# Performance work log

Hardware: AMD Instinct MI355X
Metric: run time of the kernel (lower is better)

Reference implementation:

```python
import jax, jax.numpy as jnp
import numpy as np

N = 1048576  # n_envs (patients)

# param column order in the (N,30) params array
_P = ['BW','KMAX','B','D','KMIN','KABS','F','KP1','KP2','KP3','FSNC','KE1','KE2',
     'K1','K2','VM0','VMX','KM0','M1','M2','M4','KA1','KA2','VI','P2U','IB','KI',
     'M30','KD','KSC']
_IDX = {n: i for i, n in enumerate(_P)}


def setup_inputs() -> dict:
    key = jax.random.key(0)
    ks = jax.random.split(key, 6)
    # positive, well-conditioned values (B < 1, divisors bounded away from 0)
    x = jax.random.uniform(ks[0], (N, 13), jnp.float32, 0.1, 2.0)
    params = jax.random.uniform(ks[1], (N, 30), jnp.float32, 0.5, 0.95)
    action_ins = jax.random.uniform(ks[2], (N, 1), jnp.float32, 0.0, 1.0)
    action_CHO = jax.random.uniform(ks[3], (N, 1), jnp.float32, 0.0, 1.0)
    last_Qsto = jax.random.uniform(ks[4], (N, 1), jnp.float32, 0.0, 1.0)
    last_foodtaken = jax.random.uniform(ks[5], (N, 1), jnp.float32, 0.0, 1.0)
    return {'x': x, 'params': params, 'action_ins': action_ins,
            'action_CHO': action_CHO, 'last_Qsto': last_Qsto,
            'last_foodtaken': last_foodtaken}


def _dxdt(x, params, action_ins, action_CHO, last_Qsto, last_foodtaken):
    p = lambda n: params[:, _IDX[n]:_IDX[n] + 1]  # (N,1) column
    xs = [x[:, i:i + 1] for i in range(13)]

    BW = p('BW'); KMAX = p('KMAX'); B = p('B'); D = p('D'); KMIN = p('KMIN')
    KABS = p('KABS'); F = p('F'); KP1 = p('KP1'); KP2 = p('KP2'); KP3 = p('KP3')
    FSNC = p('FSNC'); KE1 = p('KE1'); KE2 = p('KE2'); K1 = p('K1'); K2 = p('K2')
    VM0 = p('VM0'); VMX = p('VMX'); KM0 = p('KM0'); M1 = p('M1'); M2 = p('M2')
    M4 = p('M4'); KA1 = p('KA1'); KA2 = p('KA2'); VI = p('VI'); P2U = p('P2U')
    IB = p('IB'); KI = p('KI'); M30 = p('M30'); KD = p('KD'); KSC = p('KSC')

    f_insulin = action_ins * 6000.0 / BW
    qsto = xs[0] + xs[1]
    Dbar = last_Qsto + last_foodtaken

    dx0 = -KMAX * xs[0] + action_CHO * 1000.0

    aa = 5.0 / 2.0 / (1.0 - B) / (Dbar + 1e-7)
    cc = 5.0 / 2.0 / D / (Dbar + 1e-7)
    kgut_true = KMIN + (KMAX - KMIN) / 2.0 * (
        jnp.tanh(aa * (qsto - B * Dbar)) - jnp.tanh(cc * (qsto - D * Dbar)) + 2.0)
    kgut = jnp.where(Dbar > 0, kgut_true, KMAX)

    dx1 = KMAX * xs[0] - xs[1] * kgut
    dx2 = kgut * xs[1] - KABS * xs[2]

    Rat = F * KABS * xs[2] / BW
    EGPt = KP1 - KP2 * xs[3] - KP3 * xs[8]
    Et = jnp.where(xs[3] > KE2, KE1 * (xs[3] - KE2), 0.0)
    dx3 = jnp.maximum(EGPt, 0.0) + Rat - FSNC - Et - K1 * xs[3] + K2 * xs[4]
    dx3 = jnp.where(xs[3] >= 0, dx3, 0.0)

    Vmt = VM0 + VMX * xs[6]
    Uidt = Vmt * xs[4] / (KM0 + xs[4])
    dx4 = -Uidt + K1 * xs[3] - K2 * xs[4]
    dx4 = jnp.where(xs[4] >= 0, dx4, 0.0)

    dx5 = -(M2 + M4) * xs[5] + M1 * xs[9] + KA1 * xs[10] + KA2 * xs[11]
    It = xs[5] / VI
    dx5 = jnp.where(xs[5] >= 0, dx5, 0.0)

    dx6 = -P2U * xs[6] + P2U * (It - IB)
    dx7 = -KI * (xs[7] - It)
    dx8 = -KI * (xs[8] - xs[7])

    dx9 = -(M1 + M30) * xs[9] + M2 * xs[5]
    dx9 = jnp.where(xs[9] >= 0, dx9, 0.0)

    dx10 = f_insulin - (KA1 + KD) * xs[10]
    dx10 = jnp.where(xs[10] >= 0, dx10, 0.0)

    dx11 = KD * xs[10] - KA2 * xs[11]
    dx11 = jnp.where(xs[11] >= 0, dx11, 0.0)

    dx12 = -KSC * xs[12] + KSC * xs[3]
    dx12 = jnp.where(xs[12] >= 0, dx12, 0.0)

    return jnp.concatenate(
        [dx0, dx1, dx2, dx3, dx4, dx5, dx6, dx7, dx8, dx9, dx10, dx11, dx12],
        axis=1)  # (N, 13)


def reference(x, params, action_ins, action_CHO, last_Qsto, last_foodtaken):
    return _dxdt(x, params, action_ins, action_CHO, last_Qsto, last_foodtaken)
```

## Files before the change

### kernel.cpp

```cpp
#include <hip/hip_runtime.h>
#include <math.h>

#define WAVE 64
#define XW 13
#define PW 30

__device__ __forceinline__ void dxdt(const float* X, const float* P,
                                     float ai, float cho, float lq, float lf,
                                     float* dx)
{
    const float BW = P[0],  KMAX = P[1],  B   = P[2],  D   = P[3],  KMIN = P[4];
    const float KABS = P[5], F   = P[6],  KP1 = P[7],  KP2 = P[8],  KP3  = P[9];
    const float FSNC = P[10], KE1 = P[11], KE2 = P[12], K1 = P[13], K2   = P[14];
    const float VM0 = P[15], VMX = P[16], KM0 = P[17], M1 = P[18], M2   = P[19];
    const float M4  = P[20], KA1 = P[21], KA2 = P[22], VI = P[23], P2U  = P[24];
    const float IB  = P[25], KI  = P[26], M30 = P[27], KD = P[28], KSC  = P[29];

    const float f_insulin = ai * 6000.0f / BW;
    const float qsto = X[0] + X[1];
    const float Dbar = lq + lf;

    dx[0] = -KMAX * X[0] + cho * 1000.0f;

    const float inv_dbar = 1.0f / (Dbar + 1e-7f);
    const float aa = 2.5f / (1.0f - B) * inv_dbar;
    const float cc = 2.5f / D * inv_dbar;
    const float kgut_true = KMIN + (KMAX - KMIN) * 0.5f *
        (tanhf(aa * (qsto - B * Dbar)) - tanhf(cc * (qsto - D * Dbar)) + 2.0f);
    const float kgut = (Dbar > 0.0f) ? kgut_true : KMAX;

    dx[1] = KMAX * X[0] - X[1] * kgut;
    dx[2] = kgut * X[1] - KABS * X[2];

    const float Rat  = F * KABS * X[2] / BW;
    const float EGPt = KP1 - KP2 * X[3] - KP3 * X[8];
    const float Et   = (X[3] > KE2) ? KE1 * (X[3] - KE2) : 0.0f;
    const float d3 = fmaxf(EGPt, 0.0f) + Rat - FSNC - Et - K1 * X[3] + K2 * X[4];
    dx[3] = (X[3] >= 0.0f) ? d3 : 0.0f;

    const float Vmt  = VM0 + VMX * X[6];
    const float Uidt = Vmt * X[4] / (KM0 + X[4]);
    const float d4 = -Uidt + K1 * X[3] - K2 * X[4];
    dx[4] = (X[4] >= 0.0f) ? d4 : 0.0f;

    const float d5 = -(M2 + M4) * X[5] + M1 * X[9] + KA1 * X[10] + KA2 * X[11];
    const float It = X[5] / VI;
    dx[5] = (X[5] >= 0.0f) ? d5 : 0.0f;

    dx[6] = -P2U * X[6] + P2U * (It - IB);
    dx[7] = -KI * (X[7] - It);
    dx[8] = -KI * (X[8] - X[7]);

    const float d9 = -(M1 + M30) * X[9] + M2 * X[5];
    dx[9] = (X[9] >= 0.0f) ? d9 : 0.0f;

    const float d10 = f_insulin - (KA1 + KD) * X[10];
    dx[10] = (X[10] >= 0.0f) ? d10 : 0.0f;

    const float d11 = KD * X[10] - KA2 * X[11];
    dx[11] = (X[11] >= 0.0f) ? d11 : 0.0f;

    const float d12 = -KSC * X[12] + KSC * X[3];
    dx[12] = (X[12] >= 0.0f) ? d12 : 0.0f;
}

__global__ __launch_bounds__(WAVE, 4) void t1d_kernel(
    const float* __restrict__ x,
    const float* __restrict__ params,
    const float* __restrict__ action_ins,
    const float* __restrict__ action_CHO,
    const float* __restrict__ last_Qsto,
    const float* __restrict__ last_foodtaken,
    float* __restrict__ out, int n)
{
    __shared__ float xb[WAVE * XW];
    __shared__ float pb[WAVE * PW];

    const int l = threadIdx.x;
    const size_t base = (size_t)blockIdx.x * WAVE;

    if (base + WAVE <= (size_t)n) {
        const float4* xg = (const float4*)(x + base * XW);
        const float4* pg = (const float4*)(params + base * PW);
        float4* xl4 = (float4*)xb;
        float4* pl4 = (float4*)pb;

        float4 a0 = xg[l];
        float4 a1 = xg[l + 64];
        float4 a2 = xg[l + 128];
        float4 a3; if (l < 16) a3 = xg[192 + l];

        float4 b0 = pg[l];
        float4 b1 = pg[l + 64];
        float4 b2 = pg[l + 128];
        float4 b3 = pg[l + 192];
        float4 b4 = pg[l + 256];
        float4 b5 = pg[l + 320];
        float4 b6 = pg[l + 384];
        float4 b7; if (l < 32) b7 = pg[448 + l];

        const float ai  = action_ins[base + l];
        const float cho = action_CHO[base + l];
        const float lq  = last_Qsto[base + l];
        const float lf  = last_foodtaken[base + l];

        xl4[l]       = a0;
        xl4[l + 64]  = a1;
        xl4[l + 128] = a2;
        if (l < 16) xl4[192 + l] = a3;
        pl4[l]       = b0;
        pl4[l + 64]  = b1;
        pl4[l + 128] = b2;
        pl4[l + 192] = b3;
        pl4[l + 256] = b4;
        pl4[l + 320] = b5;
        pl4[l + 384] = b6;
        if (l < 32) pl4[448 + l] = b7;

        float X[XW], P[PW], dx[XW];
        #pragma unroll
        for (int j = 0; j < XW; ++j) X[j] = xb[l * XW + j];
        #pragma unroll
        for (int j = 0; j < PW; ++j) P[j] = pb[l * PW + j];

        dxdt(X, P, ai, cho, lq, lf, dx);

        #pragma unroll
        for (int j = 0; j < XW; ++j) xb[l * XW + j] = dx[j];

        float4 o0 = xl4[l];
        float4 o1 = xl4[l + 64];
        float4 o2 = xl4[l + 128];
        float4 o3; if (l < 16) o3 = xl4[192 + l];
        float4* og = (float4*)(out + base * XW);
        og[l]       = o0;
        og[l + 64]  = o1;
        og[l + 128] = o2;
        if (l < 16) og[192 + l] = o3;
    } else {
        const size_t i = base + l;
        if (i < (size_t)n) {
            float X[XW], P[PW], dx[XW];
            #pragma unroll
            for (int j = 0; j < XW; ++j) X[j] = x[i * XW + j];
            #pragma unroll
            for (int j = 0; j < PW; ++j) P[j] = params[i * PW + j];
            dxdt(X, P, action_ins[i], action_CHO[i], last_Qsto[i],
                 last_foodtaken[i], dx);
            #pragma unroll
            for (int j = 0; j < XW; ++j) out[i * XW + j] = dx[j];
        }
    }
}

extern "C" void kernel_launch(void* const* d_in, const int* in_sizes, int n_in,
                              void* d_out, int out_size, void* d_ws, size_t ws_size,
                              hipStream_t stream) {
    const float* x      = (const float*)d_in[0];
    const float* params = (const float*)d_in[1];
    const float* ai     = (const float*)d_in[2];
    const float* cho    = (const float*)d_in[3];
    const float* lq     = (const float*)d_in[4];
    const float* lf     = (const float*)d_in[5];
    float* out = (float*)d_out;

    const int n = in_sizes[0] / XW;
    const int grid = (n + WAVE - 1) / WAVE;
    t1d_kernel<<<grid, WAVE, 0, stream>>>(x, params, ai, cho, lq, lf, out, n);
}
```

Measured before the change: 247.9 us.

## Use persistent grid-stride blocks with register prefetch of next tile

Replaces one-block-per-64-patient tile with a fixed grid of 2048 single-wave blocks that loop over tiles. Each block prefetches the next tile's x, params and action vectors into registers while computing and writing the current tile, so global load latency overlaps compute. Launch bounds drop from 4 to 2 waves per EU to leave room for the doubled register footprint. The tail is now handled by a grid-stride loop. The cost is lower occupancy and fewer blocks to hide latency, on a kernel that is memory-bound.

```diff
diff --git a/kernel.cpp b/kernel.cpp
--- a/kernel.cpp
+++ b/kernel.cpp
@@ -4,6 +4,7 @@
 #define WAVE 64
 #define XW 13
 #define PW 30
+#define NBLOCK 2048
 
 __device__ __forceinline__ void dxdt(const float* X, const float* P,
                                      float ai, float cho, float lq, float lf,
@@ -64,7 +65,7 @@
     dx[12] = (X[12] >= 0.0f) ? d12 : 0.0f;
 }
 
-__global__ __launch_bounds__(WAVE, 4) void t1d_kernel(
+__global__ __launch_bounds__(WAVE, 2) void t1d_kernel(
     const float* __restrict__ x,
     const float* __restrict__ params,
     const float* __restrict__ action_ins,
@@ -73,83 +74,97 @@
     const float* __restrict__ last_foodtaken,
     float* __restrict__ out, int n)
 {
-    __shared__ float xb[WAVE * XW];
-    __shared__ float pb[WAVE * PW];
+    __shared__ __align__(16) float xb[WAVE * XW];
+    __shared__ __align__(16) float pb[WAVE * PW];
 
     const int l = threadIdx.x;
-    const size_t base = (size_t)blockIdx.x * WAVE;
+    const int ntiles = n / WAVE;
+    float4* xl4 = (float4*)xb;
+    float4* pl4 = (float4*)pb;
 
-    if (base + WAVE <= (size_t)n) {
+    int t = (int)blockIdx.x;
+    if (t < ntiles) {
+        size_t base = (size_t)t * WAVE;
         const float4* xg = (const float4*)(x + base * XW);
         const float4* pg = (const float4*)(params + base * PW);
-        float4* xl4 = (float4*)xb;
-        float4* pl4 = (float4*)pb;
+        float4 a0 = xg[l], a1 = xg[l + 64], a2 = xg[l + 128], a3;
+        if (l < 16) a3 = xg[192 + l];
+        float4 b0 = pg[l],       b1 = pg[l + 64],  b2 = pg[l + 128];
+        float4 b3 = pg[l + 192], b4 = pg[l + 256], b5 = pg[l + 320];
+        float4 b6 = pg[l + 384], b7;
+        if (l < 32) b7 = pg[448 + l];
+        float ai = action_ins[base + l], cho = action_CHO[base + l];
+        float lq = last_Qsto[base + l],  lf = last_foodtaken[base + l];
 
-        float4 a0 = xg[l];
-        float4 a1 = xg[l + 64];
-        float4 a2 = xg[l + 128];
-        float4 a3; if (l < 16) a3 = xg[192 + l];
+        #pragma clang loop unroll(disable)
+        for (;;) {
+            xl4[l]       = a0;
+            xl4[l + 64]  = a1;
+            xl4[l + 128] = a2;
+            if (l < 16) xl4[192 + l] = a3;
+            pl4[l]       = b0;
+            pl4[l + 64]  = b1;
+            pl4[l + 128] = b2;
+            pl4[l + 192] = b3;
+            pl4[l + 256] = b4;
+            pl4[l + 320] = b5;
+            pl4[l + 384] = b6;
+            if (l < 32) pl4[448 + l] = b7;
 
-        float4 b0 = pg[l];
-        float4 b1 = pg[l + 64];
-        float4 b2 = pg[l + 128];
-        float4 b3 = pg[l + 192];
-        float4 b4 = pg[l + 256];
-        float4 b5 = pg[l + 320];
-        float4 b6 = pg[l + 384];
-        float4 b7; if (l < 32) b7 = pg[448 + l];
+            const float  cai = ai, ccho = cho, clq = lq, clf = lf;
+            const size_t obase = (size_t)t * WAVE;
 
-        const float ai  = action_ins[base + l];
-        const float cho = action_CHO[base + l];
-        const float lq  = last_Qsto[base + l];
-        const float lf  = last_foodtaken[base + l];
+            const int  tn   = t + (int)gridDim.x;
+            const bool more = tn < ntiles;
+            if (more) {
+                size_t nb = (size_t)tn * WAVE;
+                const float4* xg2 = (const float4*)(x + nb * XW);
+                const float4* pg2 = (const float4*)(params + nb * PW);
+                a0 = xg2[l]; a1 = xg2[l + 64]; a2 = xg2[l + 128];
+                if (l < 16) a3 = xg2[192 + l];
+                b0 = pg2[l];       b1 = pg2[l + 64];  b2 = pg2[l + 128];
+                b3 = pg2[l + 192]; b4 = pg2[l + 256]; b5 = pg2[l + 320];
+                b6 = pg2[l + 384];
+                if (l < 32) b7 = pg2[448 + l];
+                ai = action_ins[nb + l]; cho = action_CHO[nb + l];
+                lq = last_Qsto[nb + l];  lf = last_foodtaken[nb + l];
+            }
 
-        xl4[l]       = a0;
-        xl4[l + 64]  = a1;
-        xl4[l + 128] = a2;
-        if (l < 16) xl4[192 + l] = a3;
-        pl4[l]       = b0;
-        pl4[l + 64]  = b1;
-        pl4[l + 128] = b2;
-        pl4[l + 192] = b3;
-        pl4[l + 256] = b4;
-        pl4[l + 320] = b5;
-        pl4[l + 384] = b6;
-        if (l < 32) pl4[448 + l] = b7;
+            float X[XW], P[PW], dx[XW];
+            #pragma unroll
+            for (int j = 0; j < XW; ++j) X[j] = xb[l * XW + j];
+            #pragma unroll
+            for (int j = 0; j < PW; ++j) P[j] = pb[l * PW + j];
 
+            dxdt(X, P, cai, ccho, clq, clf, dx);
+
+            #pragma unroll
+            for (int j = 0; j < XW; ++j) xb[l * XW + j] = dx[j];
+            float4 o0 = xl4[l], o1 = xl4[l + 64], o2 = xl4[l + 128], o3;
+            if (l < 16) o3 = xl4[192 + l];
+            float4* og = (float4*)(out + obase * XW);
+            og[l]       = o0;
+            og[l + 64]  = o1;
+            og[l + 128] = o2;
+            if (l < 16) og[192 + l] = o3;
+
+            if (!more) break;
+            t = tn;
+        }
+    }
+
+    const int tail0 = ntiles * WAVE;
+    for (int i = tail0 + (int)blockIdx.x * WAVE + l; i < n;
+         i += (int)gridDim.x * WAVE) {
         float X[XW], P[PW], dx[XW];
         #pragma unroll
-        for (int j = 0; j < XW; ++j) X[j] = xb[l * XW + j];
+        for (int j = 0; j < XW; ++j) X[j] = x[(size_t)i * XW + j];
         #pragma unroll
-        for (int j = 0; j < PW; ++j) P[j] = pb[l * PW + j];
-
-        dxdt(X, P, ai, cho, lq, lf, dx);
-
+        for (int j = 0; j < PW; ++j) P[j] = params[(size_t)i * PW + j];
+        dxdt(X, P, action_ins[i], action_CHO[i], last_Qsto[i],
+             last_foodtaken[i], dx);
         #pragma unroll
-        for (int j = 0; j < XW; ++j) xb[l * XW + j] = dx[j];
-
-        float4 o0 = xl4[l];
-        float4 o1 = xl4[l + 64];
-        float4 o2 = xl4[l + 128];
-        float4 o3; if (l < 16) o3 = xl4[192 + l];
-        float4* og = (float4*)(out + base * XW);
-        og[l]       = o0;
-        og[l + 64]  = o1;
-        og[l + 128] = o2;
-        if (l < 16) og[192 + l] = o3;
-    } else {
-        const size_t i = base + l;
-        if (i < (size_t)n) {
-            float X[XW], P[PW], dx[XW];
-            #pragma unroll
-            for (int j = 0; j < XW; ++j) X[j] = x[i * XW + j];
-            #pragma unroll
-            for (int j = 0; j < PW; ++j) P[j] = params[i * PW + j];
-            dxdt(X, P, action_ins[i], action_CHO[i], last_Qsto[i],
-                 last_foodtaken[i], dx);
-            #pragma unroll
-            for (int j = 0; j < XW; ++j) out[i * XW + j] = dx[j];
-        }
+        for (int j = 0; j < XW; ++j) out[(size_t)i * XW + j] = dx[j];
     }
 }
 
@@ -165,6 +180,7 @@
     float* out = (float*)d_out;
 
     const int n = in_sizes[0] / XW;
-    const int grid = (n + WAVE - 1) / WAVE;
+    const int ntiles = n / WAVE;
+    int grid = ntiles > 0 ? (ntiles < NBLOCK ? ntiles : NBLOCK) : 1;
     t1d_kernel<<<grid, WAVE, 0, stream>>>(x, params, ai, cho, lq, lf, out, n);
 }
```

New measurement: 251.5 us. Within noise of the previous version (+1.4%).
